# Kernel tuning notes

Measured on AMD Instinct MI355X. Metric: run time of the kernel, lower is better.

## Reference

```python
import jax, jax.numpy as jnp
import numpy as np

D_MODEL = 2048
D_HEAD = 128
N_HEADS = D_MODEL // D_HEAD
SEQ_LENS = (512, 768, 384, 384)  # packed varlen sequences, sum = 2048
L_TOTAL = sum(SEQ_LENS)
EPS = 1e-6


def setup_inputs() -> dict:
    key = jax.random.key(0)
    ks = jax.random.split(key, 8)
    x = jax.random.normal(ks[0], (L_TOTAL, D_MODEL), jnp.float32)
    # Flux-style rope table: pairwise-duplicated cos/sin, pe = concat([cos, sin], -1) -> (L, 2*d_head)
    half = D_HEAD // 2
    pos = np.arange(L_TOTAL, dtype=np.float32)[:, None]
    freqs = 1.0 / (10000.0 ** (np.arange(half, dtype=np.float32) / half))  # (half,)
    ang = pos * freqs[None, :]                      # (L, half)
    cos = np.repeat(np.cos(ang), 2, axis=-1)        # (L, d_head), duplicated per pair
    sin = np.repeat(np.sin(ang), 2, axis=-1)
    pe = jnp.asarray(np.concatenate([cos, sin], axis=-1))  # (L, 2*d_head)
    seq_lens = jnp.asarray(SEQ_LENS, dtype=jnp.int32)
    std = 0.02
    qkv_w = std * jax.random.truncated_normal(ks[1], -2.0, 2.0, (3 * D_MODEL, D_MODEL), jnp.float32)
    qkv_b = jnp.zeros((3 * D_MODEL,), jnp.float32)
    q_scale = jnp.ones((D_HEAD,), jnp.float32)
    k_scale = jnp.ones((D_HEAD,), jnp.float32)
    proj_w = std * jax.random.truncated_normal(ks[2], -2.0, 2.0, (D_MODEL, D_MODEL), jnp.float32)
    proj_b = jnp.zeros((D_MODEL,), jnp.float32)
    return {"x": x, "pe": pe, "seq_lens": seq_lens, "qkv_w": qkv_w, "qkv_b": qkv_b,
            "q_scale": q_scale, "k_scale": k_scale, "proj_w": proj_w, "proj_b": proj_b}


def _rms_norm(t, scale):
    tf = t.astype(jnp.float32)
    rrms = jax.lax.rsqrt(jnp.mean(tf * tf, axis=-1, keepdims=True) + EPS)
    return (tf * rrms * scale).astype(t.dtype)


def _apply_rope(t, pe):
    # t: (L, nh, dh); pe: (L, 2*dh) with pairwise-duplicated cos|sin
    L, nh, dh = t.shape
    c = pe[:, None, 0:dh:2]     # (L, 1, dh/2) per-pair cos
    s = pe[:, None, dh::2]      # (L, 1, dh/2) per-pair sin
    tr = t.reshape(L, nh, dh // 2, 2)
    t1, t2 = tr[..., 0], tr[..., 1]
    out = jnp.stack([t1 * c - t2 * s, t1 * s + t2 * c], axis=-1)
    return out.reshape(L, nh, dh)


def reference(x, pe, seq_lens, qkv_w, qkv_b, q_scale, k_scale, proj_w, proj_b):
    L = x.shape[0]
    qkv = x @ qkv_w.T + qkv_b                      # (L, 3*D)
    q, k, v = jnp.split(qkv, 3, axis=-1)
    q = q.reshape(L, N_HEADS, D_HEAD)
    k = k.reshape(L, N_HEADS, D_HEAD)
    v = v.reshape(L, N_HEADS, D_HEAD)
    q = _rms_norm(q, q_scale)
    k = _rms_norm(k, k_scale)
    q = _apply_rope(q, pe)
    k = _apply_rope(k, pe)
    # block-diagonal (packed varlen) attention
    n = seq_lens.shape[0]
    seg = jnp.repeat(jnp.arange(n, dtype=jnp.int32), seq_lens, total_repeat_length=L)  # (L,)
    mask = seg[:, None] == seg[None, :]            # (L, L) block-diagonal
    scale = 1.0 / jnp.sqrt(jnp.float32(D_HEAD))
    scores = jnp.einsum('lhd,mhd->hlm', q, k) * scale  # (nh, L, L)
    scores = jnp.where(mask[None], scores, jnp.finfo(scores.dtype).min)
    p = jax.nn.softmax(scores, axis=-1)
    out = jnp.einsum('hlm,mhd->lhd', p, v)         # (L, nh, dh)
    out = out.reshape(L, D_MODEL)
    return out @ proj_w.T + proj_b
```

## Files before the change

kernel.cpp:

```cpp
#include <hip/hip_runtime.h>

typedef unsigned short ushort_t;
typedef __attribute__((ext_vector_type(4))) float f4;
typedef __attribute__((ext_vector_type(8))) short s8v;
typedef __attribute__((ext_vector_type(8))) __bf16 bf8v;

#define AS1 __attribute__((address_space(1)))
#define AS3 __attribute__((address_space(3)))

__device__ __forceinline__ void async16(void* lds, const void* g) {
    __builtin_amdgcn_global_load_lds((AS1 const void*)g, (AS3 void*)lds, 16, 0, 0);
}

__device__ __forceinline__ f4 mfma16(s8v a, s8v b, f4 c) {
    return __builtin_amdgcn_mfma_f32_16x16x32_bf16(
        __builtin_bit_cast(bf8v, a), __builtin_bit_cast(bf8v, b), c, 0, 0, 0);
}

__device__ __forceinline__ ushort_t f2bf(float f) {
    unsigned int u = __float_as_uint(f);
    u += 0x7fffu + ((u >> 16) & 1u);
    return (ushort_t)(u >> 16);
}
__device__ __forceinline__ float bf2f(ushort_t u) {
    return __uint_as_float(((unsigned int)u) << 16);
}

#define L_TOT   2048
#define DMODEL  2048
#define DHEAD   128
#define NHEADS  16

__global__ __launch_bounds__(256) void cast_all(const float* __restrict__ x,
                                                const float* __restrict__ w1,
                                                const float* __restrict__ w2,
                                                ushort_t* __restrict__ xo,
                                                ushort_t* __restrict__ w1o,
                                                ushort_t* __restrict__ w2o) {
    int i = blockIdx.x * 256 + threadIdx.x;
    const float* src; ushort_t* dst; int off;
    if (i < 1048576)      { src = x;  dst = xo;  off = 0; }
    else if (i < 4194304) { src = w1; dst = w1o; off = 1048576; }
    else                  { src = w2; dst = w2o; off = 4194304; }
    int j = i - off;
    float4 v = ((const float4*)src)[j];
    ushort4 o;
    o.x = f2bf(v.x); o.y = f2bf(v.y); o.z = f2bf(v.z); o.w = f2bf(v.w);
    ((ushort4*)dst)[j] = o;
}


template <int P>
__device__ __forceinline__ void cluster(f4 (&acc)[8][4], const s8v (&af)[2][2],
                                        const s8v (&bf)[4][2]) {
    __builtin_amdgcn_s_setprio(1);
#pragma unroll
    for (int mm = 0; mm < 2; mm++)
#pragma unroll
        for (int nn = 0; nn < 4; nn++) {
            acc[2 * P + mm][nn] = mfma16(af[mm][0], bf[nn][0], acc[2 * P + mm][nn]);
            acc[2 * P + mm][nn] = mfma16(af[mm][1], bf[nn][1], acc[2 * P + mm][nn]);
        }
    __builtin_amdgcn_s_setprio(0);
}

#define LDF(base, row, oo) (*(const s8v*)&(base)[(row) * 64 + (oo)])

#define STG(dst, gb, Tt, h)                                                              \
    async16(&(dst)[tid * 8 + (2 * (h)) * 4096],                                          \
            (gb) + (size_t)(Tt) * 64 + (size_t)(128 * (h)) * K);                         \
    async16(&(dst)[tid * 8 + (2 * (h) + 1) * 4096],                                      \
            (gb) + (size_t)(Tt) * 64 + (size_t)(128 * (h) + 64) * K);

#define OPENB()                                                                          \
    __builtin_amdgcn_s_barrier();                                                        \
    asm volatile("s_waitcnt lgkmcnt(0)" ::: "memory");                                   \
    __builtin_amdgcn_sched_barrier(0);

#define TILE(cur, T)                                                                     \
    {                                                                                    \
        const int Tn1 = ((T) + 1 < NT) ? (T) + 1 : NT - 1;                               \
        const int Tn2 = ((T) + 2 < NT) ? (T) + 2 : NT - 1;                               \
        const ushort_t* fA = stA[cur];                                                   \
        const ushort_t* fB = stB[cur];                                                   \
        s8v bfrag[4][2];                                                                 \
        s8v afrag[2][2];                                                                 \
                                                                  \
        bfrag[0][0] = LDF(fB, brow + 0,  o0); bfrag[0][1] = LDF(fB, brow + 0,  o1);      \
        bfrag[1][0] = LDF(fB, brow + 16, o0); bfrag[1][1] = LDF(fB, brow + 16, o1);      \
        bfrag[2][0] = LDF(fB, brow + 32, o0); bfrag[2][1] = LDF(fB, brow + 32, o1);      \
        bfrag[3][0] = LDF(fB, brow + 48, o0); bfrag[3][1] = LDF(fB, brow + 48, o1);      \
        afrag[0][0] = LDF(fA, arow + 0,  o0); afrag[0][1] = LDF(fA, arow + 0,  o1);      \
        afrag[1][0] = LDF(fA, arow + 16, o0); afrag[1][1] = LDF(fA, arow + 16, o1);      \
        STG(stA[(cur) ^ 1], gA, Tn1, 0)                                                  \
        OPENB()                                                                          \
        cluster<0>(acc, afrag, bfrag);                                                   \
        __builtin_amdgcn_s_barrier();                                                    \
                                                                  \
        afrag[0][0] = LDF(fA, arow + 32, o0); afrag[0][1] = LDF(fA, arow + 32, o1);      \
        afrag[1][0] = LDF(fA, arow + 48, o0); afrag[1][1] = LDF(fA, arow + 48, o1);      \
        STG(stA[(cur) ^ 1], gA, Tn1, 1)                                                  \
        OPENB()                                                                          \
        cluster<1>(acc, afrag, bfrag);                                                   \
        __builtin_amdgcn_s_barrier();                                                    \
                                                                  \
        afrag[0][0] = LDF(fA, arow + 64, o0); afrag[0][1] = LDF(fA, arow + 64, o1);      \
        afrag[1][0] = LDF(fA, arow + 80, o0); afrag[1][1] = LDF(fA, arow + 80, o1);      \
        STG(stB[cur], gB, Tn2, 0)                                                        \
        OPENB()                                                                          \
        cluster<2>(acc, afrag, bfrag);                                                   \
        __builtin_amdgcn_s_barrier();                                                    \
                                                                  \
        afrag[0][0] = LDF(fA, arow + 96,  o0); afrag[0][1] = LDF(fA, arow + 96,  o1);    \
        afrag[1][0] = LDF(fA, arow + 112, o0); afrag[1][1] = LDF(fA, arow + 112, o1);    \
        STG(stB[cur], gB, Tn2, 1)                                                        \
        asm volatile("s_waitcnt vmcnt(4)" ::: "memory");                                 \
        __builtin_amdgcn_sched_barrier(0);                                               \
        OPENB()                                                                          \
        cluster<3>(acc, afrag, bfrag);                                                   \
        __builtin_amdgcn_s_barrier();                                                    \
    }

__global__ __launch_bounds__(512, 2) void gemm_qkv256(const ushort_t* __restrict__ A,
                                                      const ushort_t* __restrict__ Bt,
                                                      const float* __restrict__ bias,
                                                      ushort_t* __restrict__ qk_out,
                                                      ushort_t* __restrict__ vt_out,
                                                      int K) {
    __shared__ alignas(16) ushort_t sA[2][16384];
    __shared__ alignas(16) ushort_t sB[2][16384];

    const int tid  = threadIdx.x;
    const int lane = tid & 63;
    const int wave = tid >> 6;
    const int wm = wave >> 2;
    const int wn = wave & 3;

    const int phys = blockIdx.y * 8 + blockIdx.x;
    const int lid  = (phys & 7) * 24 + (phys >> 3);
    const int bxs  = lid & 7;
    const int bys  = lid >> 3;

    const int bm = bxs * 256;
    const int bn = bys * 256;
    const bool is_v = bys >= 16;
    const int NT = K >> 6;

    const int q15 = lane & 15;
    const int g   = lane >> 4;
    const int l7  = lane & 7;
    const int o0  = ((g    ) ^ l7) * 8;
    const int o1  = ((g + 4) ^ l7) * 8;
    const int arow = wm * 128 + q15;
    const int brow = wn * 64 + q15;

    const int rs  = tid >> 3;
    const int csw = ((tid & 7) ^ (rs & 7)) * 8;
    const ushort_t* Abase = A  + (size_t)(bm + rs) * K + csw;
    const ushort_t* Bbase = Bt + (size_t)(bn + rs) * K + csw;

    ushort_t* stA[2]; ushort_t* stB[2];
    const ushort_t* gA; const ushort_t* gB;
    if (!is_v) { stA[0] = sA[0]; stA[1] = sA[1]; stB[0] = sB[0]; stB[1] = sB[1];
                 gA = Abase; gB = Bbase; }
    else       { stA[0] = sB[0]; stA[1] = sB[1]; stB[0] = sA[0]; stB[1] = sA[1];
                 gA = Bbase; gB = Abase; }

    f4 acc[8][4];
#pragma unroll
    for (int i = 0; i < 8; i++)
#pragma unroll
        for (int j = 0; j < 4; j++) acc[i][j] = (f4){0.f, 0.f, 0.f, 0.f};

    STG(stA[0], gA, 0, 0) STG(stA[0], gA, 0, 1)
    STG(stB[0], gB, 0, 0) STG(stB[0], gB, 0, 1)
    {
        const int T1 = NT > 1 ? 1 : 0;
        STG(stB[1], gB, T1, 0) STG(stB[1], gB, T1, 1)
    }
    asm volatile("s_waitcnt vmcnt(4)" ::: "memory");
    __builtin_amdgcn_sched_barrier(0);
    __builtin_amdgcn_s_barrier();

    for (int T = 0; T < NT; T += 2) {
        TILE(0, T)
        TILE(1, T + 1)
    }

    if (!is_v) {
#pragma unroll
        for (int n = 0; n < 4; n++) {
            int col = bn + wn * 64 + n * 16 + q15;
            float bv = bias[col];
#pragma unroll
            for (int m = 0; m < 8; m++) {
                int r0 = bm + wm * 128 + m * 16 + g * 4;
#pragma unroll
                for (int r = 0; r < 4; r++)
                    qk_out[(size_t)(r0 + r) * 4096 + col] = f2bf(acc[m][n][r] + bv);
            }
        }
    } else {
        const int cb   = (bys - 16) * 256 + wm * 128;
        const int tok0 = bm + wn * 64 + q15;
#pragma unroll
        for (int m = 0; m < 8; m++) {
#pragma unroll
            for (int r = 0; r < 4; r++) {
                int c = cb + m * 16 + g * 4 + r;
                float bv = bias[4096 + c];
#pragma unroll
                for (int n = 0; n < 4; n++)
                    vt_out[(size_t)c * L_TOT + tok0 + n * 16] = f2bf(acc[m][n][r] + bv);
            }
        }
    }
}

__global__ __launch_bounds__(256) void gemm_proj(const ushort_t* __restrict__ A,
                                                 const ushort_t* __restrict__ Bt,
                                                 const float* __restrict__ bias,
                                                 float* __restrict__ out,
                                                 int K) {
    __shared__ alignas(16) ushort_t pA[128 * 64];
    __shared__ alignas(16) ushort_t pB[128 * 64];
    const int tid  = threadIdx.x;
    const int lane = tid & 63;
    const int wave = tid >> 6;
    const int wr = (wave >> 1) * 64;
    const int wc = (wave & 1) * 64;

    const int phys = blockIdx.y * 16 + blockIdx.x;
    const int lid  = (phys & 7) * 32 + (phys >> 3);
    const int bm = (lid & 15) * 128;
    const int bn = (lid >> 4) * 128;

    f4 acc[4][4];
#pragma unroll
    for (int i = 0; i < 4; i++)
#pragma unroll
        for (int j = 0; j < 4; j++) acc[i][j] = (f4){0.f, 0.f, 0.f, 0.f};

    const int rs  = tid >> 3;
    const int csw = ((tid & 7) ^ (rs & 7)) * 8;
    const ushort_t* Abase = A  + (size_t)(bm + rs) * K + csw;
    const ushort_t* Bbase = Bt + (size_t)(bn + rs) * K + csw;
    const int arow = wr + (lane & 15);
    const int brow = wc + (lane & 15);
    const int l7 = lane & 7;
    const int o0 = (((lane >> 4)    ) ^ l7) * 8;
    const int o1 = (((lane >> 4) + 4) ^ l7) * 8;

    for (int k0 = 0; k0 < K; k0 += 64) {
#pragma unroll
        for (int s = 0; s < 4; s++) {
            async16(&pA[tid * 8 + s * 2048], Abase + k0 + (size_t)(32 * s) * K);
            async16(&pB[tid * 8 + s * 2048], Bbase + k0 + (size_t)(32 * s) * K);
        }
        __syncthreads();

        s8v af[4], bfr[4];
#pragma unroll
        for (int i = 0; i < 4; i++) af[i]  = *(const s8v*)&pA[(arow + i * 16) * 64 + o0];
#pragma unroll
        for (int j = 0; j < 4; j++) bfr[j] = *(const s8v*)&pB[(brow + j * 16) * 64 + o0];
#pragma unroll
        for (int i = 0; i < 4; i++)
#pragma unroll
            for (int j = 0; j < 4; j++) acc[i][j] = mfma16(af[i], bfr[j], acc[i][j]);

#pragma unroll
        for (int i = 0; i < 4; i++) af[i]  = *(const s8v*)&pA[(arow + i * 16) * 64 + o1];
#pragma unroll
        for (int j = 0; j < 4; j++) bfr[j] = *(const s8v*)&pB[(brow + j * 16) * 64 + o1];
#pragma unroll
        for (int i = 0; i < 4; i++)
#pragma unroll
            for (int j = 0; j < 4; j++) acc[i][j] = mfma16(af[i], bfr[j], acc[i][j]);
        __syncthreads();
    }

    const int q = lane & 15;
    const int g = lane >> 4;
    const int crow0 = bm + wr + g * 4;
    const int ccol0 = bn + wc + q;
#pragma unroll
    for (int j = 0; j < 4; j++) {
        int col = ccol0 + j * 16;
        float bv = bias[col];
#pragma unroll
        for (int i = 0; i < 4; i++) {
#pragma unroll
            for (int r = 0; r < 4; r++)
                out[(size_t)(crow0 + i * 16 + r) * DMODEL + col] = acc[i][j][r] + bv;
        }
    }
}

__global__ __launch_bounds__(256) void norm_rope(const ushort_t* __restrict__ qk,
                                                 const float* __restrict__ pe,
                                                 const float* __restrict__ q_scale,
                                                 const float* __restrict__ k_scale,
                                                 ushort_t* __restrict__ qh,
                                                 ushort_t* __restrict__ kh) {
    int wid  = blockIdx.x * 4 + (threadIdx.x >> 6);
    int lane = threadIdx.x & 63;
    int l = wid >> 4;
    int h = wid & 15;

    const ushort_t* base = qk + (size_t)l * 4096 + h * DHEAD + 2 * lane;
    ushort2 qu = *(const ushort2*)base;
    ushort2 ku = *(const ushort2*)(base + 2048);
    float qvx = bf2f(qu.x), qvy = bf2f(qu.y);
    float kvx = bf2f(ku.x), kvy = bf2f(ku.y);

    float qss = qvx * qvx + qvy * qvy;
    float kss = kvx * kvx + kvy * kvy;
#pragma unroll
    for (int m = 32; m >= 1; m >>= 1) {
        qss += __shfl_xor(qss, m);
        kss += __shfl_xor(kss, m);
    }
    float qr = rsqrtf(qss * (1.0f / DHEAD) + 1e-6f);
    float kr = rsqrtf(kss * (1.0f / DHEAD) + 1e-6f);

    float c = pe[(size_t)l * 256 + 2 * lane];
    float s = pe[(size_t)l * 256 + 128 + 2 * lane];

    float q1 = qvx * qr * q_scale[2 * lane];
    float q2 = qvy * qr * q_scale[2 * lane + 1];
    float k1 = kvx * kr * k_scale[2 * lane];
    float k2 = kvy * kr * k_scale[2 * lane + 1];

    const float sc = 0.08838834764831845f;
    float qo0 = (q1 * c - q2 * s) * sc;
    float qo1 = (q1 * s + q2 * c) * sc;
    float ko0 = k1 * c - k2 * s;
    float ko1 = k1 * s + k2 * c;

    size_t o = ((size_t)h * L_TOT + l) * DHEAD + 2 * lane;
    ushort2 qp, kp;
    qp.x = f2bf(qo0); qp.y = f2bf(qo1);
    kp.x = f2bf(ko0); kp.y = f2bf(ko1);
    *(ushort2*)(qh + o) = qp;
    *(ushort2*)(kh + o) = kp;
}

__global__ __launch_bounds__(256) void attn_kernel(const ushort_t* __restrict__ qh,
                                                   const ushort_t* __restrict__ kh,
                                                   const ushort_t* __restrict__ vt,
                                                   ushort_t* __restrict__ attn_out) {
    __shared__ alignas(16) ushort_t sK[64 * 128];
    __shared__ alignas(16) ushort_t sV[128 * 64];
    __shared__ alignas(16) ushort_t sP[4][16 * 64];

    const int phys = blockIdx.y * 32 + blockIdx.x;
    const int lid  = (phys & 7) * 64 + (phys >> 3);
    const int qt = lid & 31;
    const int h  = lid >> 5;

    const int tid = threadIdx.x;
    const int lane = tid & 63;
    const int w = tid >> 6;
    const int qrow0 = qt * 64 + w * 16;

    int q0 = qt * 64;
    int seg_start, seg_end;
    if (q0 < 512)       { seg_start = 0;    seg_end = 512;  }
    else if (q0 < 1280) { seg_start = 512;  seg_end = 1280; }
    else if (q0 < 1664) { seg_start = 1280; seg_end = 1664; }
    else                { seg_start = 1664; seg_end = 2048; }

    const int g = lane >> 4;
    const int q = lane & 15;
    const int qa7 = q & 7;

    const ushort_t* ksrc[4];
    const ushort_t* vsrc[4];
#pragma unroll
    for (int i = 0; i < 4; i++) {
        int p = i * 256 + tid;
        ksrc[i] = kh + ((size_t)h * L_TOT + (p >> 4)) * DHEAD + ((p & 15) ^ ((p >> 4) & 7)) * 8;
        vsrc[i] = vt + ((size_t)h * DHEAD + (p >> 3)) * L_TOT + ((p & 7) ^ ((p >> 3) & 7)) * 8;
    }

    s8v qf[4];
    {
        const ushort_t* qbase = qh + ((size_t)h * L_TOT + qrow0 + q) * DHEAD;
#pragma unroll
        for (int kd = 0; kd < 4; kd++) qf[kd] = *(const s8v*)(qbase + kd * 32 + g * 8);
    }

    f4 o[8];
#pragma unroll
    for (int j = 0; j < 8; j++) o[j] = (f4){0.f, 0.f, 0.f, 0.f};
    float lsum[4] = {0.f, 0.f, 0.f, 0.f};

    for (int kt = seg_start; kt < seg_end; kt += 64) {
#pragma unroll
        for (int i = 0; i < 4; i++) {
            int p = i * 256 + tid;
            async16(&sK[p * 8], ksrc[i] + (size_t)kt * DHEAD);
            async16(&sV[p * 8], vsrc[i] + kt);
        }
        __syncthreads();

        f4 S[4];
#pragma unroll
        for (int tj = 0; tj < 4; tj++) {
            f4 st = (f4){0.f, 0.f, 0.f, 0.f};
#pragma unroll
            for (int kd = 0; kd < 4; kd++) {
                s8v bfrag = *(const s8v*)&sK[(tj * 16 + q) * 128 + (((kd * 4 + g) ^ qa7) * 8)];
                st = mfma16(qf[kd], bfrag, st);
            }
            S[tj] = st;
        }

#pragma unroll
        for (int tj = 0; tj < 4; tj++)
#pragma unroll
            for (int r = 0; r < 4; r++) {
                float p = __expf(S[tj][r]);
                S[tj][r] = p;
                lsum[r] += p;
            }

#pragma unroll
        for (int tj = 0; tj < 4; tj++) {
            int cg = tj * 2 + (q >> 3);
#pragma unroll
            for (int r = 0; r < 4; r++) {
                int prow = g * 4 + r;
                sP[w][prow * 64 + ((cg ^ (prow & 7)) * 8) + qa7] = f2bf(S[tj][r]);
            }
        }
        asm volatile("s_waitcnt lgkmcnt(0)" ::: "memory");

#pragma unroll
        for (int ks = 0; ks < 2; ks++) {
            s8v pf = *(const s8v*)&sP[w][q * 64 + (((ks * 4 + g) ^ qa7) * 8)];
#pragma unroll
            for (int j = 0; j < 8; j++) {
                s8v vf = *(const s8v*)&sV[(j * 16 + q) * 64 + (((ks * 4 + g) ^ qa7) * 8)];
                o[j] = mfma16(pf, vf, o[j]);
            }
        }
        __syncthreads();
    }

#pragma unroll
    for (int r = 0; r < 4; r++) {
        float rs = lsum[r];
        rs += __shfl_xor(rs, 1);
        rs += __shfl_xor(rs, 2);
        rs += __shfl_xor(rs, 4);
        rs += __shfl_xor(rs, 8);
        int row = qrow0 + g * 4 + r;
        float inv = 1.0f / rs;
#pragma unroll
        for (int j = 0; j < 8; j++) {
            attn_out[(size_t)row * DMODEL + h * DHEAD + j * 16 + q] = f2bf(o[j][r] * inv);
        }
    }
}

extern "C" void kernel_launch(void* const* d_in, const int* in_sizes, int n_in,
                              void* d_out, int out_size, void* d_ws, size_t ws_size,
                              hipStream_t stream) {
    const float* x       = (const float*)d_in[0];
    const float* pe      = (const float*)d_in[1];
    const float* qkv_w   = (const float*)d_in[3];
    const float* qkv_b   = (const float*)d_in[4];
    const float* q_scale = (const float*)d_in[5];
    const float* k_scale = (const float*)d_in[6];
    const float* proj_w  = (const float*)d_in[7];
    const float* proj_b  = (const float*)d_in[8];
    float* out = (float*)d_out;

    char* ws = (char*)d_ws;
    const size_t MB = 1024 * 1024;
    ushort_t* x_bf     = (ushort_t*)(ws + 0);
    ushort_t* wqkv_bf  = (ushort_t*)(ws + 8 * MB);
    ushort_t* wproj_bf = (ushort_t*)(ws + 32 * MB);
    ushort_t* qk_bf    = (ushort_t*)(ws + 40 * MB);
    ushort_t* qh       = (ushort_t*)(ws + 57 * MB);
    ushort_t* kh       = (ushort_t*)(ws + 65 * MB);
    ushort_t* vt       = (ushort_t*)(ws + 73 * MB);
    ushort_t* attn_b   = (ushort_t*)(ws + 81 * MB);

    cast_all<<<20480, 256, 0, stream>>>(x, qkv_w, proj_w, x_bf, wqkv_bf, wproj_bf);

    gemm_qkv256<<<dim3(8, 24), 512, 0, stream>>>(x_bf, wqkv_bf, qkv_b, qk_bf, vt, 2048);

    norm_rope<<<8192, 256, 0, stream>>>(qk_bf, pe, q_scale, k_scale, qh, kh);

    attn_kernel<<<dim3(32, 16), 256, 0, stream>>>(qh, kh, vt, attn_b);

    gemm_proj<<<dim3(16, 16), 256, 0, stream>>>(attn_b, wproj_bf, proj_b, out, 2048);
}
```

Baseline: 262.0 us.

## Triple-buffer A in QKV GEMM and split-K the projection GEMM with reduce

The QKV GEMM moves from double to triple buffering of the A tile (plus double-buffered B) in a single 160KB LDS allocation. Loads are prefetched two tiles ahead, and the wait on outstanding loads is moved after the last MFMA cluster. This drops occupancy to one block per CU to hide global latency better. Separately, the projection GEMM is split along K into two halves writing fp32 partials, followed by a reduce kernel that sums them and adds the bias. This doubles the block count for better CU fill, at the cost of extra partial-buffer traffic and a launch.

```diff
diff --git a/kernel.cpp b/kernel.cpp
--- a/kernel.cpp
+++ b/kernel.cpp
@@ -77,58 +77,54 @@
     asm volatile("s_waitcnt lgkmcnt(0)" ::: "memory");                                   \
     __builtin_amdgcn_sched_barrier(0);
 
-#define TILE(cur, T)                                                                     \
+#define TILE(T)                                                                          \
     {                                                                                    \
-        const int Tn1 = ((T) + 1 < NT) ? (T) + 1 : NT - 1;                               \
-        const int Tn2 = ((T) + 2 < NT) ? (T) + 2 : NT - 1;                               \
-        const ushort_t* fA = stA[cur];                                                   \
-        const ushort_t* fB = stB[cur];                                                   \
+        const int Tp2 = ((T) + 2 < NT) ? (T) + 2 : NT - 1;                               \
         s8v bfrag[4][2];                                                                 \
         s8v afrag[2][2];                                                                 \
                                                                   \
-        bfrag[0][0] = LDF(fB, brow + 0,  o0); bfrag[0][1] = LDF(fB, brow + 0,  o1);      \
-        bfrag[1][0] = LDF(fB, brow + 16, o0); bfrag[1][1] = LDF(fB, brow + 16, o1);      \
-        bfrag[2][0] = LDF(fB, brow + 32, o0); bfrag[2][1] = LDF(fB, brow + 32, o1);      \
-        bfrag[3][0] = LDF(fB, brow + 48, o0); bfrag[3][1] = LDF(fB, brow + 48, o1);      \
-        afrag[0][0] = LDF(fA, arow + 0,  o0); afrag[0][1] = LDF(fA, arow + 0,  o1);      \
-        afrag[1][0] = LDF(fA, arow + 16, o0); afrag[1][1] = LDF(fA, arow + 16, o1);      \
-        STG(stA[(cur) ^ 1], gA, Tn1, 0)                                                  \
+        bfrag[0][0] = LDF(b0, brow + 0,  o0); bfrag[0][1] = LDF(b0, brow + 0,  o1);      \
+        bfrag[1][0] = LDF(b0, brow + 16, o0); bfrag[1][1] = LDF(b0, brow + 16, o1);      \
+        bfrag[2][0] = LDF(b0, brow + 32, o0); bfrag[2][1] = LDF(b0, brow + 32, o1);      \
+        bfrag[3][0] = LDF(b0, brow + 48, o0); bfrag[3][1] = LDF(b0, brow + 48, o1);      \
+        afrag[0][0] = LDF(a0, arow + 0,  o0); afrag[0][1] = LDF(a0, arow + 0,  o1);      \
+        afrag[1][0] = LDF(a0, arow + 16, o0); afrag[1][1] = LDF(a0, arow + 16, o1);      \
+        STG(a2, gA, Tp2, 0)                                                              \
         OPENB()                                                                          \
         cluster<0>(acc, afrag, bfrag);                                                   \
         __builtin_amdgcn_s_barrier();                                                    \
                                                                   \
-        afrag[0][0] = LDF(fA, arow + 32, o0); afrag[0][1] = LDF(fA, arow + 32, o1);      \
-        afrag[1][0] = LDF(fA, arow + 48, o0); afrag[1][1] = LDF(fA, arow + 48, o1);      \
-        STG(stA[(cur) ^ 1], gA, Tn1, 1)                                                  \
+        afrag[0][0] = LDF(a0, arow + 32, o0); afrag[0][1] = LDF(a0, arow + 32, o1);      \
+        afrag[1][0] = LDF(a0, arow + 48, o0); afrag[1][1] = LDF(a0, arow + 48, o1);      \
+        STG(a2, gA, Tp2, 1)                                                              \
         OPENB()                                                                          \
         cluster<1>(acc, afrag, bfrag);                                                   \
         __builtin_amdgcn_s_barrier();                                                    \
                                                                   \
-        afrag[0][0] = LDF(fA, arow + 64, o0); afrag[0][1] = LDF(fA, arow + 64, o1);      \
-        afrag[1][0] = LDF(fA, arow + 80, o0); afrag[1][1] = LDF(fA, arow + 80, o1);      \
-        STG(stB[cur], gB, Tn2, 0)                                                        \
+        afrag[0][0] = LDF(a0, arow + 64, o0); afrag[0][1] = LDF(a0, arow + 64, o1);      \
+        afrag[1][0] = LDF(a0, arow + 80, o0); afrag[1][1] = LDF(a0, arow + 80, o1);      \
+        STG(b0, gB, Tp2, 0)                                                              \
         OPENB()                                                                          \
         cluster<2>(acc, afrag, bfrag);                                                   \
         __builtin_amdgcn_s_barrier();                                                    \
                                                                   \
-        afrag[0][0] = LDF(fA, arow + 96,  o0); afrag[0][1] = LDF(fA, arow + 96,  o1);    \
-        afrag[1][0] = LDF(fA, arow + 112, o0); afrag[1][1] = LDF(fA, arow + 112, o1);    \
-        STG(stB[cur], gB, Tn2, 1)                                                        \
-        asm volatile("s_waitcnt vmcnt(4)" ::: "memory");                                 \
-        __builtin_amdgcn_sched_barrier(0);                                               \
+        afrag[0][0] = LDF(a0, arow + 96,  o0); afrag[0][1] = LDF(a0, arow + 96,  o1);    \
+        afrag[1][0] = LDF(a0, arow + 112, o0); afrag[1][1] = LDF(a0, arow + 112, o1);    \
+        STG(b0, gB, Tp2, 1)                                                              \
         OPENB()                                                                          \
         cluster<3>(acc, afrag, bfrag);                                                   \
+        asm volatile("s_waitcnt vmcnt(8)" ::: "memory");                                 \
+        __builtin_amdgcn_sched_barrier(0);                                               \
         __builtin_amdgcn_s_barrier();                                                    \
     }
 
-__global__ __launch_bounds__(512, 2) void gemm_qkv256(const ushort_t* __restrict__ A,
+__global__ __launch_bounds__(512, 1) void gemm_qkv256(const ushort_t* __restrict__ A,
                                                       const ushort_t* __restrict__ Bt,
                                                       const float* __restrict__ bias,
                                                       ushort_t* __restrict__ qk_out,
                                                       ushort_t* __restrict__ vt_out,
                                                       int K) {
-    __shared__ alignas(16) ushort_t sA[2][16384];
-    __shared__ alignas(16) ushort_t sB[2][16384];
+    __shared__ alignas(16) ushort_t lds[5 * 16384];
 
     const int tid  = threadIdx.x;
     const int lane = tid & 63;
@@ -159,12 +155,14 @@
     const ushort_t* Abase = A  + (size_t)(bm + rs) * K + csw;
     const ushort_t* Bbase = Bt + (size_t)(bn + rs) * K + csw;
 
-    ushort_t* stA[2]; ushort_t* stB[2];
-    const ushort_t* gA; const ushort_t* gB;
-    if (!is_v) { stA[0] = sA[0]; stA[1] = sA[1]; stB[0] = sB[0]; stB[1] = sB[1];
-                 gA = Abase; gB = Bbase; }
-    else       { stA[0] = sB[0]; stA[1] = sB[1]; stB[0] = sA[0]; stB[1] = sA[1];
-                 gA = Bbase; gB = Abase; }
+    const ushort_t* gA = is_v ? Bbase : Abase;
+    const ushort_t* gB = is_v ? Abase : Bbase;
+
+    ushort_t* a0 = lds;
+    ushort_t* a1 = lds + 16384;
+    ushort_t* a2 = lds + 32768;
+    ushort_t* b0 = lds + 49152;
+    ushort_t* b1 = lds + 65536;
 
     f4 acc[8][4];
 #pragma unroll
@@ -172,19 +170,21 @@
 #pragma unroll
         for (int j = 0; j < 4; j++) acc[i][j] = (f4){0.f, 0.f, 0.f, 0.f};
 
-    STG(stA[0], gA, 0, 0) STG(stA[0], gA, 0, 1)
-    STG(stB[0], gB, 0, 0) STG(stB[0], gB, 0, 1)
     {
         const int T1 = NT > 1 ? 1 : 0;
-        STG(stB[1], gB, T1, 0) STG(stB[1], gB, T1, 1)
-    }
-    asm volatile("s_waitcnt vmcnt(4)" ::: "memory");
+        STG(a0, gA, 0, 0) STG(a0, gA, 0, 1)
+        STG(b0, gB, 0, 0) STG(b0, gB, 0, 1)
+        STG(a1, gA, T1, 0) STG(a1, gA, T1, 1)
+        STG(b1, gB, T1, 0) STG(b1, gB, T1, 1)
+    }
+    asm volatile("s_waitcnt vmcnt(8)" ::: "memory");
     __builtin_amdgcn_sched_barrier(0);
     __builtin_amdgcn_s_barrier();
 
-    for (int T = 0; T < NT; T += 2) {
-        TILE(0, T)
-        TILE(1, T + 1)
+    for (int T = 0; T < NT; T++) {
+        TILE(T)
+        ushort_t* t = a0; a0 = a1; a1 = a2; a2 = t;
+        t = b0; b0 = b1; b1 = t;
     }
 
     if (!is_v) {
@@ -219,8 +219,7 @@
 
 __global__ __launch_bounds__(256) void gemm_proj(const ushort_t* __restrict__ A,
                                                  const ushort_t* __restrict__ Bt,
-                                                 const float* __restrict__ bias,
-                                                 float* __restrict__ out,
+                                                 float* __restrict__ Cf,
                                                  int K) {
     __shared__ alignas(16) ushort_t pA[128 * 64];
     __shared__ alignas(16) ushort_t pB[128 * 64];
@@ -229,11 +228,8 @@
     const int wave = tid >> 6;
     const int wr = (wave >> 1) * 64;
     const int wc = (wave & 1) * 64;
-
-    const int phys = blockIdx.y * 16 + blockIdx.x;
-    const int lid  = (phys & 7) * 32 + (phys >> 3);
-    const int bm = (lid & 15) * 128;
-    const int bn = (lid >> 4) * 128;
+    const int bm = blockIdx.x * 128;
+    const int bn = blockIdx.y * 128;
 
     f4 acc[4][4];
 #pragma unroll
@@ -250,8 +246,10 @@
     const int l7 = lane & 7;
     const int o0 = (((lane >> 4)    ) ^ l7) * 8;
     const int o1 = (((lane >> 4) + 4) ^ l7) * 8;
-
-    for (int k0 = 0; k0 < K; k0 += 64) {
+    const int kbeg = blockIdx.z * (K >> 1);
+    const int kend = kbeg + (K >> 1);
+
+    for (int k0 = kbeg; k0 < kend; k0 += 64) {
 #pragma unroll
         for (int s = 0; s < 4; s++) {
             async16(&pA[tid * 8 + s * 2048], Abase + k0 + (size_t)(32 * s) * K);
@@ -284,17 +282,27 @@
     const int g = lane >> 4;
     const int crow0 = bm + wr + g * 4;
     const int ccol0 = bn + wc + q;
+    float* Cp = Cf + (size_t)blockIdx.z * L_TOT * DMODEL;
 #pragma unroll
     for (int j = 0; j < 4; j++) {
         int col = ccol0 + j * 16;
-        float bv = bias[col];
 #pragma unroll
         for (int i = 0; i < 4; i++) {
 #pragma unroll
             for (int r = 0; r < 4; r++)
-                out[(size_t)(crow0 + i * 16 + r) * DMODEL + col] = acc[i][j][r] + bv;
-        }
-    }
+                Cp[(size_t)(crow0 + i * 16 + r) * DMODEL + col] = acc[i][j][r];
+        }
+    }
+}
+
+__global__ __launch_bounds__(256) void reduce_bias(const float* __restrict__ part,
+                                                   const float* __restrict__ bias,
+                                                   float* __restrict__ out) {
+    int i = blockIdx.x * 256 + threadIdx.x;
+    f4 a = ((const f4*)part)[i];
+    f4 b = ((const f4*)(part + (size_t)L_TOT * DMODEL))[i];
+    f4 bv = ((const f4*)bias)[i & 511];
+    ((f4*)out)[i] = a + b + bv;
 }
 
 __global__ __launch_bounds__(256) void norm_rope(const ushort_t* __restrict__ qk,
@@ -488,6 +496,7 @@
     ushort_t* kh       = (ushort_t*)(ws + 65 * MB);
     ushort_t* vt       = (ushort_t*)(ws + 73 * MB);
     ushort_t* attn_b   = (ushort_t*)(ws + 81 * MB);
+    float*    part     = (float*)   (ws + 40 * MB);
 
     cast_all<<<20480, 256, 0, stream>>>(x, qkv_w, proj_w, x_bf, wqkv_bf, wproj_bf);
 
@@ -497,5 +506,6 @@
 
     attn_kernel<<<dim3(32, 16), 256, 0, stream>>>(qh, kh, vt, attn_b);
 
-    gemm_proj<<<dim3(16, 16), 256, 0, stream>>>(attn_b, wproj_bf, proj_b, out, 2048);
-}
+    gemm_proj<<<dim3(16, 16, 2), 256, 0, stream>>>(attn_b, wproj_bf, part, 2048);
+    reduce_bias<<<4096, 256, 0, stream>>>(part, proj_b, out);
+}
```

Measured after the change: 258.2 us. About the same (-1.4%).
